# Performance work log

Hardware: AMD Instinct MI355X
Metric: run time of the kernel (lower is better)

## Reference

```python
import jax, jax.numpy as jnp
import numpy as np

B, S, E, H = 2, 2048, 2048, 16
NOPE, ROPE, VD = 128, 64, 128
QH = NOPE + ROPE  # 192
LORA = 512
ROPE_THETA = 10000.0
EPS = 1e-6


def setup_inputs() -> dict:
    key = jax.random.key(0)
    ks = jax.random.split(key, 5)
    sd = lambda n: 1.0 / np.sqrt(n)
    return {
        "x": jax.random.normal(ks[0], (B, S, E), jnp.float32),
        "wq": jax.random.normal(ks[1], (E, H * QH), jnp.float32) * sd(E),
        "wkv_a": jax.random.normal(ks[2], (E, LORA + ROPE), jnp.float32) * sd(E),
        "wkv_b": jax.random.normal(ks[3], (LORA, H * (NOPE + VD)), jnp.float32) * sd(LORA),
        "wo": jax.random.normal(ks[4], (H * VD, E), jnp.float32) * sd(H * VD),
        "kv_norm_scale": jnp.ones((LORA,), jnp.float32),
    }


def _rope(xp, cos, sin):
    # xp: (..., s, d); cos/sin: (s, d//2)
    d2 = xp.shape[-1] // 2
    x1, x2 = xp[..., :d2], xp[..., d2:]
    return jnp.concatenate([x1 * cos - x2 * sin, x2 * cos + x1 * sin], axis=-1)


def reference(x, wq, wkv_a, wkv_b, wo, kv_norm_scale):
    b, s, _ = x.shape
    # queries: (b, H, s, QH), split into no-pe / pe slices
    q = (x @ wq).reshape(b, s, H, QH).transpose(0, 2, 1, 3)
    q_nope, q_pe = q[..., :NOPE], q[..., NOPE:]

    # low-rank KV latent projection
    kva = x @ wkv_a  # (b, s, LORA + ROPE)
    ckv, k_pe = kva[..., :LORA], kva[..., LORA:]
    ckv = ckv * jax.lax.rsqrt(jnp.mean(ckv * ckv, axis=-1, keepdims=True) + EPS)
    ckv = ckv * kv_norm_scale  # RMSNorm on latent
    kv = (ckv @ wkv_b).reshape(b, s, H, NOPE + VD).transpose(0, 2, 1, 3)
    k_nope, v = kv[..., :NOPE], kv[..., NOPE:]

    # partial RoPE on the rope slice only
    pos = jnp.arange(s, dtype=jnp.float32)
    inv = 1.0 / (ROPE_THETA ** (jnp.arange(0, ROPE, 2, dtype=jnp.float32) / ROPE))
    ang = pos[:, None] * inv  # (s, ROPE//2)
    cos, sin = jnp.cos(ang), jnp.sin(ang)
    q_pe = _rope(q_pe, cos, sin)                 # (b, H, s, ROPE)
    k_pe = _rope(k_pe[:, None, :, :], cos, sin)  # (b, 1, s, ROPE), shared over heads

    # concat (the new_empty + slice-write in torch)
    qs = jnp.concatenate([q_nope, q_pe], axis=-1)  # (b, H, s, QH)
    ks_ = jnp.concatenate(
        [k_nope, jnp.broadcast_to(k_pe, (b, H, s, ROPE))], axis=-1
    )  # (b, H, s, QH)

    # causal SDPA with scale = q_head_dim**-0.5; asymmetric V head dim
    scale = QH ** -0.5
    scores = jnp.einsum('bhqd,bhkd->bhqk', qs, ks_) * scale
    causal = jnp.tril(jnp.ones((s, s), dtype=bool))
    scores = jnp.where(causal, scores, jnp.finfo(scores.dtype).min)
    attn = jax.nn.softmax(scores, axis=-1)
    out = jnp.einsum('bhqk,bhkd->bhqd', attn, v)  # (b, H, s, VD)
    out = out.transpose(0, 2, 1, 3).reshape(b, s, H * VD)
    return out @ wo
```

## Files before the change

### kernel.cpp

```cpp
#include <hip/hip_runtime.h>
#include <stdint.h>
#include <stddef.h>

typedef __bf16 bf16x8 __attribute__((ext_vector_type(8)));
typedef float floatx4 __attribute__((ext_vector_type(4)));
typedef unsigned short u16;

__device__ __forceinline__ float bf2f(u16 h) {
    unsigned u = ((unsigned)h) << 16;
    return __builtin_bit_cast(float, u);
}
__device__ __forceinline__ u16 f2bf(float f) {
    unsigned u = __builtin_bit_cast(unsigned, f);
    u += 0x7fffu + ((u >> 16) & 1u);
    return (u16)(u >> 16);
}

__device__ __forceinline__ void gload16(const void* g, void* l) {
    __builtin_amdgcn_global_load_lds(
        (const __attribute__((address_space(1))) uint32_t*)g,
        (__attribute__((address_space(3))) uint32_t*)l, 16, 0, 0);
}

__device__ __forceinline__ void wait_vm8() { asm volatile("s_waitcnt vmcnt(8)" ::: "memory"); }
__device__ __forceinline__ void wait_vm6() { asm volatile("s_waitcnt vmcnt(6)" ::: "memory"); }
__device__ __forceinline__ void wait_vm4() { asm volatile("s_waitcnt vmcnt(4)" ::: "memory"); }
__device__ __forceinline__ void wait_vm3() { asm volatile("s_waitcnt vmcnt(3)" ::: "memory"); }
__device__ __forceinline__ void wait_vm0() { asm volatile("s_waitcnt vmcnt(0)" ::: "memory"); }

__global__ __launch_bounds__(256) void k_conv_x(const float* __restrict__ in,
                                                u16* __restrict__ out, int n8) {
    int i = blockIdx.x * 256 + threadIdx.x;
    if (i >= n8) return;
    const float* f = in + (size_t)i * 8;
    unsigned o[4];
    for (int t = 0; t < 4; t++) {
        u16 lo = f2bf(f[2 * t]), hi = f2bf(f[2 * t + 1]);
        o[t] = (unsigned)lo | ((unsigned)hi << 16);
    }
    uint4 p = {o[0], o[1], o[2], o[3]};
    *(uint4*)&out[(size_t)i * 8] = p;
}

__global__ __launch_bounds__(256) void k_convT(const float* __restrict__ in,
                                               u16* __restrict__ out, int K, int N) {
    __shared__ u16 t[32][33];
    int k0 = blockIdx.x * 32, n0 = blockIdx.y * 32;
    int c = threadIdx.x & 31, r8 = threadIdx.x >> 5;
    for (int j = 0; j < 4; j++) {
        int row = r8 + j * 8;
        int n = n0 + c;
        t[row][c] = (n < N) ? f2bf(in[(size_t)(k0 + row) * N + n]) : (u16)0;
    }
    __syncthreads();
    for (int j = 0; j < 4; j++) {
        int row = r8 + j * 8;
        out[(size_t)(n0 + row) * K + k0 + c] = t[c][row];
    }
}

__global__ __launch_bounds__(256) void k_transpose_v(const u16* __restrict__ kv,
                                                     u16* __restrict__ vt) {
    __shared__ u16 t[32][33];
    int bh = blockIdx.z;
    int s0 = blockIdx.x * 32, v0 = blockIdx.y * 32;
    int c = threadIdx.x & 31, r8 = threadIdx.x >> 5;
    int b = bh >> 4, h = bh & 15;
    for (int j = 0; j < 4; j++) {
        int s = s0 + r8 + j * 8;
        t[r8 + j * 8][c] = kv[(size_t)(b * 2048 + s) * 4096 + h * 256 + 128 + v0 + c];
    }
    __syncthreads();
    for (int j = 0; j < 4; j++) {
        int v = v0 + r8 + j * 8;
        vt[((size_t)bh * 128 + v) * 2048 + s0 + c] = t[c][r8 + j * 8];
    }
}

template <bool F32OUT>
__global__ __launch_bounds__(256) void k_gemm_bt(const u16* __restrict__ A,
                                                 const u16* __restrict__ BT,
                                                 void* __restrict__ Cout,
                                                 int N, int K, int ldc) {
    __shared__ __align__(16) u16 As[128 * 32];
    __shared__ __align__(16) u16 Bs[128 * 32];
    int tid = threadIdx.x;
    int lane = tid & 63, wave = tid >> 6;
    int quad = lane >> 4, l15 = lane & 15;
    size_t m0 = (size_t)blockIdx.x * 128, n0 = (size_t)blockIdx.y * 128;
    int wm = (wave >> 1) * 64, wn = (wave & 1) * 64;
    const floatx4 fzero = {0.f, 0.f, 0.f, 0.f};
    floatx4 acc[4][4];
    for (int i = 0; i < 4; i++)
        for (int j = 0; j < 4; j++) acc[i][j] = fzero;

    for (int k0 = 0; k0 < K; k0 += 32) {
        for (int i = 0; i < 2; i++) {
            int cid = i * 256 + wave * 64 + lane;
            int row = cid >> 2, kc = cid & 3;
            gload16(&A[(m0 + row) * K + k0 + kc * 8], &As[(size_t)(i * 256 + wave * 64) * 8]);
            gload16(&BT[(n0 + row) * K + k0 + kc * 8], &Bs[(size_t)(i * 256 + wave * 64) * 8]);
        }
        __syncthreads();
        bf16x8 af[4], bfr[4];
        for (int i = 0; i < 4; i++) af[i]  = *(const bf16x8*)&As[(wm + i * 16 + l15) * 32 + quad * 8];
        for (int j = 0; j < 4; j++) bfr[j] = *(const bf16x8*)&Bs[(wn + j * 16 + l15) * 32 + quad * 8];
        for (int i = 0; i < 4; i++)
            for (int j = 0; j < 4; j++)
                acc[i][j] = __builtin_amdgcn_mfma_f32_16x16x32_bf16(af[i], bfr[j], acc[i][j], 0, 0, 0);
        __syncthreads();
    }
    for (int i = 0; i < 4; i++)
        for (int j = 0; j < 4; j++) {
            int col = (int)n0 + wn + j * 16 + l15;
            if (col >= N) continue;
            for (int r = 0; r < 4; r++) {
                size_t row = m0 + wm + i * 16 + quad * 4 + r;
                if (F32OUT) ((float*)Cout)[row * ldc + col] = acc[i][j][r];
                else        ((u16*)Cout)[row * ldc + col] = f2bf(acc[i][j][r]);
            }
        }
}

template <int NWC, bool F32OUT>
__global__ __launch_bounds__(512, 2) void k_gemm256(const u16* __restrict__ A,
                                                    const u16* __restrict__ BT,
                                                    void* __restrict__ Cout,
                                                    int K, int ldc) {
    constexpr int MFR = 16 / (8 / NWC);
    constexpr int ACH = 2;
    constexpr int BCH = NWC / 2;
    constexpr int SLOT = 8192 + NWC * 2048;
    __shared__ __align__(16) u16 RING[4][SLOT];
    int tid = threadIdx.x;
    int w = tid >> 6, lane = tid & 63;
    int l15 = lane & 15, quad = lane >> 4;
    int wr = w / NWC, wc = w % NWC;

    int gx = gridDim.x;
    int nwg = gx * gridDim.y;
    int flat = blockIdx.y * gx + blockIdx.x;
    int cpx = nwg >> 3;
    int swz = (flat & 7) * cpx + (flat >> 3);
    int bx = swz % gx, by = swz / gx;
    size_t m0 = (size_t)bx * 256, n0 = (size_t)by * (NWC * 64);
    int NT = K >> 5;

    const u16* srcA[ACH];
    const u16* srcB[BCH];
    int ldsAb[ACH], ldsBb[BCH];
#pragma unroll
    for (int p = 0; p < ACH; p++) {
        int chunk = p * 512 + tid;
        int s = chunk >> 6;
        int b = (chunk & 63) * 8;
        int bu = b ^ (((b >> 8) & 1) << 4);
        int r = bu >> 5, c = bu & 31;
        srcA[p] = A + (m0 + s * 16 + r) * (size_t)K + c;
        ldsAb[p] = (p * 512 + w * 64) * 8;
    }
#pragma unroll
    for (int p = 0; p < BCH; p++) {
        int chunk = p * 512 + tid;
        int s = chunk >> 6;
        int b = (chunk & 63) * 8;
        int bu = b ^ (((b >> 8) & 1) << 4);
        int r = bu >> 5, c = bu & 31;
        srcB[p] = BT + (n0 + s * 16 + r) * (size_t)K + c;
        ldsBb[p] = 8192 + (p * 512 + w * 64) * 8;
    }

    const int swb = (l15 * 32 + quad * 8) ^ ((l15 >> 3) << 4);

    floatx4 acc[MFR][4];
    const floatx4 fzero = {0.f, 0.f, 0.f, 0.f};
#pragma unroll
    for (int i = 0; i < MFR; i++)
#pragma unroll
        for (int j = 0; j < 4; j++) acc[i][j] = fzero;

    bf16x8 aA[MFR], bB[4];

    auto STAGE = [&](int j) {
        int rs = j & 3;
        size_t ko = (size_t)j * 32;
        u16* ring = &RING[rs][0];
#pragma unroll
        for (int p = 0; p < ACH; p++) gload16(srcA[p] + ko, ring + ldsAb[p]);
#pragma unroll
        for (int p = 0; p < BCH; p++) gload16(srcB[p] + ko, ring + ldsBb[p]);
    };
    auto READ = [&](int rs) {
        const u16* ring = &RING[rs][0];
#pragma unroll
        for (int i2 = 0; i2 < MFR; i2++)
            aA[i2] = *(const bf16x8*)&ring[(wr * MFR + i2) * 512 + swb];
#pragma unroll
        for (int j2 = 0; j2 < 4; j2++)
            bB[j2] = *(const bf16x8*)&ring[8192 + (wc * 4 + j2) * 512 + swb];
    };
    auto MMA = [&]() {
        __builtin_amdgcn_s_setprio(1);
#pragma unroll
        for (int i2 = 0; i2 < MFR; i2++)
#pragma unroll
            for (int j2 = 0; j2 < 4; j2++)
                acc[i2][j2] = __builtin_amdgcn_mfma_f32_16x16x32_bf16(
                    aA[i2], bB[j2], acc[i2][j2], 0, 0, 0);
        __builtin_amdgcn_s_setprio(0);
    };

    STAGE(0); STAGE(1); STAGE(2);

    int j = 0;
    for (; j + 3 < NT; j++) {
        if constexpr (NWC == 4) wait_vm8(); else wait_vm6();
        __builtin_amdgcn_s_barrier();
        __builtin_amdgcn_sched_barrier(0);
        READ(j & 3);
        STAGE(j + 3);
        __builtin_amdgcn_sched_barrier(0);
        MMA();
    }
    {
        if constexpr (NWC == 4) wait_vm8(); else wait_vm6();
        __builtin_amdgcn_s_barrier();
        __builtin_amdgcn_sched_barrier(0);
        READ(j & 3); MMA(); j++;
    }
    {
        if constexpr (NWC == 4) wait_vm4(); else wait_vm3();
        __builtin_amdgcn_s_barrier();
        __builtin_amdgcn_sched_barrier(0);
        READ(j & 3); MMA(); j++;
    }
    {
        wait_vm0();
        __builtin_amdgcn_s_barrier();
        __builtin_amdgcn_sched_barrier(0);
        READ(j & 3); MMA();
    }

#pragma unroll
    for (int i = 0; i < MFR; i++)
#pragma unroll
        for (int j2 = 0; j2 < 4; j2++) {
            size_t col = n0 + wc * 64 + j2 * 16 + l15;
#pragma unroll
            for (int r = 0; r < 4; r++) {
                size_t row = m0 + (size_t)wr * (MFR * 16) + i * 16 + quad * 4 + r;
                if (F32OUT) ((float*)Cout)[row * ldc + col] = acc[i][j2][r];
                else        ((u16*)Cout)[row * ldc + col] = f2bf(acc[i][j2][r]);
            }
        }
}

__global__ __launch_bounds__(64) void k_rmsnorm(const u16* __restrict__ kva,
                                                const float* __restrict__ scl,
                                                u16* __restrict__ ckv) {
    int r = blockIdx.x, lane = threadIdx.x;
    const u16* row = kva + (size_t)r * 576 + lane * 8;
    uint4 raw = *(const uint4*)row;
    unsigned w[4] = {raw.x, raw.y, raw.z, raw.w};
    float f[8];
    float ss = 0.f;
    for (int t = 0; t < 4; t++) {
        f[2 * t]     = bf2f((u16)(w[t] & 0xffffu));
        f[2 * t + 1] = bf2f((u16)(w[t] >> 16));
        ss += f[2 * t] * f[2 * t] + f[2 * t + 1] * f[2 * t + 1];
    }
    for (int off = 1; off < 64; off <<= 1) ss += __shfl_xor(ss, off, 64);
    float rs = rsqrtf(ss * (1.f / 512.f) + 1e-6f);
    unsigned o[4];
    for (int t = 0; t < 4; t++) {
        u16 lo = f2bf(f[2 * t] * rs * scl[lane * 8 + 2 * t]);
        u16 hi = f2bf(f[2 * t + 1] * rs * scl[lane * 8 + 2 * t + 1]);
        o[t] = (unsigned)lo | ((unsigned)hi << 16);
    }
    uint4 packed = {o[0], o[1], o[2], o[3]};
    *(uint4*)(ckv + (size_t)r * 512 + lane * 8) = packed;
}

__global__ __launch_bounds__(256) void k_rope(u16* __restrict__ qbuf, u16* __restrict__ kva) {
    int tid = threadIdx.x;
    int rloc = tid >> 7;
    int task = tid & 127;
    int r = blockIdx.x * 2 + rloc;
    __shared__ float cs_s[2][32], sn_s[2][32];
    if (tid < 64) {
        int rr = tid >> 5, i = tid & 31;
        int ss = (blockIdx.x * 2 + rr) & 2047;
        float freq = __expf(-0.28782313662425575f * (float)i);
        float ang = (float)ss * freq;
        float sn, cs;
        sincosf(ang, &sn, &cs);
        cs_s[rr][i] = cs; sn_s[rr][i] = sn;
    }
    __syncthreads();
    if (task < 68) {
        int rb = task >> 2, q = task & 3;
        u16* base = (rb < 16) ? qbuf + (size_t)r * 3072 + rb * 192 + 128
                              : kva + (size_t)r * 576 + 512;
        u16* p1 = base + q * 8;
        uint4 x1v = *(uint4*)p1;
        uint4 x2v = *(uint4*)(p1 + 32);
        unsigned w1[4] = {x1v.x, x1v.y, x1v.z, x1v.w};
        unsigned w2[4] = {x2v.x, x2v.y, x2v.z, x2v.w};
        unsigned o1[4], o2[4];
        for (int t2 = 0; t2 < 4; t2++) {
            float a1 = bf2f((u16)(w1[t2] & 0xffffu)), b1 = bf2f((u16)(w1[t2] >> 16));
            float a2 = bf2f((u16)(w2[t2] & 0xffffu)), b2 = bf2f((u16)(w2[t2] >> 16));
            int i0 = q * 8 + t2 * 2, i1 = i0 + 1;
            float c0 = cs_s[rloc][i0], s0 = sn_s[rloc][i0];
            float c1 = cs_s[rloc][i1], s1 = sn_s[rloc][i1];
            o1[t2] = (unsigned)f2bf(a1 * c0 - a2 * s0) | ((unsigned)f2bf(b1 * c1 - b2 * s1) << 16);
            o2[t2] = (unsigned)f2bf(a2 * c0 + a1 * s0) | ((unsigned)f2bf(b2 * c1 + b1 * s1) << 16);
        }
        uint4 y1 = {o1[0], o1[1], o1[2], o1[3]};
        uint4 y2 = {o2[0], o2[1], o2[2], o2[3]};
        *(uint4*)p1 = y1;
        *(uint4*)(p1 + 32) = y2;
    }
}

__global__ __launch_bounds__(256, 3) void k_attn(const u16* __restrict__ qbuf,
                                                 const u16* __restrict__ kv,
                                                 const u16* __restrict__ kva,
                                                 const u16* __restrict__ vt,
                                                 u16* __restrict__ attno) {
    int tid = threadIdx.x;
    int wave = tid >> 6, lane = tid & 63;
    int quad = lane >> 4, l15 = lane & 15;
    int hb = blockIdx.x;
    int h = hb & 15, b = hb >> 4;
    int qb = 31 - (int)blockIdx.y;
    int qg0 = qb * 64 + wave * 16;
    int row = qg0 + l15;

    __shared__ __align__(16) u16 Kn[2][32 * 136];
    __shared__ __align__(16) u16 Kp[2][32 * 72];
    __shared__ __align__(16) u16 Vs[2][128 * 40];
    __shared__ __align__(16) u16 P[4][16 * 40];

    const u16* qrp = qbuf + ((size_t)(b * 2048) + qg0 + l15) * 3072 + h * 192;
    bf16x8 qf[6];
    for (int c = 0; c < 6; c++) qf[c] = *(const bf16x8*)&qrp[c * 32 + quad * 8];

    const floatx4 fzero = {0.f, 0.f, 0.f, 0.f};
    floatx4 o[8];
    for (int f = 0; f < 8; f++) o[f] = fzero;
    float lp = 0.f;

    const u16* kvb = kv  + (size_t)(b * 2048) * 4096 + h * 256;
    const u16* kpb = kva + (size_t)(b * 2048) * 576 + 512;
    const u16* vtb = vt  + (size_t)(b * 16 + h) * 128 * 2048;
    const float scale = 0.07216878364870323f;

    int nkt = qb * 2 + 2;

    int kKey0 = tid >> 4,          kOff0 = (tid & 15) * 8;
    int kKey1 = (tid + 256) >> 4,  kOff1 = (tid & 15) * 8;
    int pKey  = tid >> 3,          pOff  = (tid & 7) * 8;
    int vRow0 = tid >> 2,          vOff0 = (tid & 3) * 8;
    int vRow1 = (tid + 256) >> 2,  vOff1 = (tid & 3) * 8;

    {
        uint4 a = *(const uint4*)&kvb[(size_t)kKey0 * 4096 + kOff0];
        uint4 c = *(const uint4*)&kvb[(size_t)kKey1 * 4096 + kOff1];
        uint4 d = *(const uint4*)&kpb[(size_t)pKey * 576 + pOff];
        uint4 e = *(const uint4*)&vtb[(size_t)vRow0 * 2048 + vOff0];
        uint4 g = *(const uint4*)&vtb[(size_t)vRow1 * 2048 + vOff1];
        *(uint4*)&Kn[0][kKey0 * 136 + kOff0] = a;
        *(uint4*)&Kn[0][kKey1 * 136 + kOff1] = c;
        *(uint4*)&Kp[0][pKey * 72 + pOff] = d;
        *(uint4*)&Vs[0][vRow0 * 40 + vOff0] = e;
        *(uint4*)&Vs[0][vRow1 * 40 + vOff1] = g;
    }
    __syncthreads();

    for (int kt = 0; kt < nkt; kt++) {
        int cur = kt & 1;
        bool have = (kt + 1) < nkt;
        uint4 sA = {}, sB = {}, sC = {}, sD = {}, sE = {};
        if (have) {
            int kb = (kt + 1) * 32;
            sA = *(const uint4*)&kvb[(size_t)(kb + kKey0) * 4096 + kOff0];
            sB = *(const uint4*)&kvb[(size_t)(kb + kKey1) * 4096 + kOff1];
            sC = *(const uint4*)&kpb[(size_t)(kb + pKey) * 576 + pOff];
            sD = *(const uint4*)&vtb[(size_t)vRow0 * 2048 + kb + vOff0];
            sE = *(const uint4*)&vtb[(size_t)vRow1 * 2048 + kb + vOff1];
        }
        if (kt * 32 <= qg0 + 15) {
            bf16x8 vf[8];
            for (int f = 0; f < 8; f++)
                vf[f] = *(const bf16x8*)&Vs[cur][(f * 16 + l15) * 40 + quad * 8];
            floatx4 sc[2] = {fzero, fzero};
            for (int hf = 0; hf < 2; hf++) {
                const u16* kn = &Kn[cur][(hf * 16 + l15) * 136];
                const u16* kp = &Kp[cur][(hf * 16 + l15) * 72];
                for (int c = 0; c < 4; c++) {
                    bf16x8 kf = *(const bf16x8*)&kn[c * 32 + quad * 8];
                    sc[hf] = __builtin_amdgcn_mfma_f32_16x16x32_bf16(kf, qf[c], sc[hf], 0, 0, 0);
                }
                for (int c = 0; c < 2; c++) {
                    bf16x8 kf = *(const bf16x8*)&kp[c * 32 + quad * 8];
                    sc[hf] = __builtin_amdgcn_mfma_f32_16x16x32_bf16(kf, qf[4 + c], sc[hf], 0, 0, 0);
                }
            }
            asm volatile("" ::: "memory");
            for (int hf = 0; hf < 2; hf++) {
                int keyb = kt * 32 + hf * 16 + quad * 4;
                float p[4];
                for (int r = 0; r < 4; r++)
                    p[r] = (keyb + r <= row) ? __expf(sc[hf][r] * scale) : 0.f;
                lp += (p[0] + p[1]) + (p[2] + p[3]);
                unsigned d0 = (unsigned)f2bf(p[0]) | ((unsigned)f2bf(p[1]) << 16);
                unsigned d1 = (unsigned)f2bf(p[2]) | ((unsigned)f2bf(p[3]) << 16);
                uint2 pk = {d0, d1};
                *(uint2*)&P[wave][l15 * 40 + hf * 16 + quad * 4] = pk;
            }
            asm volatile("" ::: "memory");
            bf16x8 pa = *(const bf16x8*)&P[wave][l15 * 40 + quad * 8];
            asm volatile("" ::: "memory");
            for (int f = 0; f < 8; f++)
                o[f] = __builtin_amdgcn_mfma_f32_16x16x32_bf16(pa, vf[f], o[f], 0, 0, 0);
        }
        if (have) {
            int nb = cur ^ 1;
            *(uint4*)&Kn[nb][kKey0 * 136 + kOff0] = sA;
            *(uint4*)&Kn[nb][kKey1 * 136 + kOff1] = sB;
            *(uint4*)&Kp[nb][pKey * 72 + pOff] = sC;
            *(uint4*)&Vs[nb][vRow0 * 40 + vOff0] = sD;
            *(uint4*)&Vs[nb][vRow1 * 40 + vOff1] = sE;
        }
        __syncthreads();
    }

    lp += __shfl_xor(lp, 16, 64);
    lp += __shfl_xor(lp, 32, 64);
    float lrow[4];
    for (int r = 0; r < 4; r++) lrow[r] = __shfl(lp, quad * 4 + r, 64);
    for (int f = 0; f < 8; f++)
        for (int r = 0; r < 4; r++) {
            int orow = qg0 + quad * 4 + r;
            float val = o[f][r] / lrow[r];
            attno[((size_t)(b * 2048) + orow) * 2048 + h * 128 + f * 16 + l15] = f2bf(val);
        }
}

extern "C" void kernel_launch(void* const* d_in, const int* in_sizes, int n_in,
                              void* d_out, int out_size, void* d_ws, size_t ws_size,
                              hipStream_t stream) {
    const float* x_raw    = (const float*)d_in[0];
    const float* wq_raw   = (const float*)d_in[1];
    const float* wkva_raw = (const float*)d_in[2];
    const float* wkvb_raw = (const float*)d_in[3];
    const float* wo_raw   = (const float*)d_in[4];
    const float* kvs_raw  = (const float*)d_in[5];
    float* out = (float*)d_out;
    u16* ws = (u16*)d_ws;

    const size_t O_ATT = 0;
    const size_t O_VT  = 8388608;
    const size_t O_QB  = 16777216;
    const size_t O_KVA = 29360128;
    const size_t O_KV  = 31719424;
    const size_t TOTAL_BYTES = 48496640ull * 2;
    if (ws_size < TOTAL_BYTES) return;

    u16* wq_t   = ws + O_ATT;
    u16* wkva_t = ws + O_ATT;
    u16* ckv    = ws + O_ATT;
    u16* wkvb_t = ws + O_ATT + 2097152;
    u16* attno  = ws + O_ATT;
    u16* x_bf   = ws + O_VT;
    u16* vt     = ws + O_VT;
    u16* qbuf   = ws + O_QB;
    u16* wo_t   = ws + O_QB;
    u16* kva    = ws + O_KVA;
    u16* kv     = ws + O_KV;

    k_conv_x<<<4096, 256, 0, stream>>>(x_raw, x_bf, 1048576);
    k_convT<<<dim3(64, 96), 256, 0, stream>>>(wq_raw, wq_t, 2048, 3072);

    k_gemm256<4, false><<<dim3(16, 12), 512, 0, stream>>>(x_bf, wq_t, qbuf, 2048, 3072);

    k_convT<<<dim3(64, 20), 256, 0, stream>>>(wkva_raw, wkva_t, 2048, 576);
    k_gemm_bt<false><<<dim3(32, 5), 256, 0, stream>>>(x_bf, wkva_t, kva, 576, 2048, 576);

    k_rmsnorm<<<4096, 64, 0, stream>>>(kva, kvs_raw, ckv);
    k_convT<<<dim3(16, 128), 256, 0, stream>>>(wkvb_raw, wkvb_t, 512, 4096);
    k_gemm256<4, false><<<dim3(16, 16), 512, 0, stream>>>(ckv, wkvb_t, kv, 512, 4096);

    k_rope<<<2048, 256, 0, stream>>>(qbuf, kva);
    k_transpose_v<<<dim3(64, 4, 32), 256, 0, stream>>>(kv, vt);

    k_attn<<<dim3(32, 32), 256, 0, stream>>>(qbuf, kv, kva, vt, attno);

    k_convT<<<dim3(64, 64), 256, 0, stream>>>(wo_raw, wo_t, 2048, 2048);
    k_gemm256<2, true><<<dim3(16, 16), 512, 0, stream>>>(attno, wo_t, out, 2048, 2048);
}
```

Before: 404.7 us.

## Fuse Q and KV-A projections into one GEMM; raise MFMA priority in attention

The transposed Wq and Wkv_a weights are stacked into one 3648-column B matrix. A single pipelined 256-row GEMM now produces both outputs, with an epilogue that routes columns to qbuf or kva. This drops the separate unpipelined 128-tile kernel for the KV-A projection and one launch, at the cost of running the Q part at a narrower column tile and computing a padded tail tile whose results are thrown away. Separately, the attention kernel wraps its QK and PV MFMA blocks in s_setprio so those waves get issue priority over waves doing loads and softmax.

```diff
diff --git a/kernel.cpp b/kernel.cpp
--- a/kernel.cpp
+++ b/kernel.cpp
@@ -77,55 +77,11 @@
     }
 }
 
-template <bool F32OUT>
-__global__ __launch_bounds__(256) void k_gemm_bt(const u16* __restrict__ A,
-                                                 const u16* __restrict__ BT,
-                                                 void* __restrict__ Cout,
-                                                 int N, int K, int ldc) {
-    __shared__ __align__(16) u16 As[128 * 32];
-    __shared__ __align__(16) u16 Bs[128 * 32];
-    int tid = threadIdx.x;
-    int lane = tid & 63, wave = tid >> 6;
-    int quad = lane >> 4, l15 = lane & 15;
-    size_t m0 = (size_t)blockIdx.x * 128, n0 = (size_t)blockIdx.y * 128;
-    int wm = (wave >> 1) * 64, wn = (wave & 1) * 64;
-    const floatx4 fzero = {0.f, 0.f, 0.f, 0.f};
-    floatx4 acc[4][4];
-    for (int i = 0; i < 4; i++)
-        for (int j = 0; j < 4; j++) acc[i][j] = fzero;
-
-    for (int k0 = 0; k0 < K; k0 += 32) {
-        for (int i = 0; i < 2; i++) {
-            int cid = i * 256 + wave * 64 + lane;
-            int row = cid >> 2, kc = cid & 3;
-            gload16(&A[(m0 + row) * K + k0 + kc * 8], &As[(size_t)(i * 256 + wave * 64) * 8]);
-            gload16(&BT[(n0 + row) * K + k0 + kc * 8], &Bs[(size_t)(i * 256 + wave * 64) * 8]);
-        }
-        __syncthreads();
-        bf16x8 af[4], bfr[4];
-        for (int i = 0; i < 4; i++) af[i]  = *(const bf16x8*)&As[(wm + i * 16 + l15) * 32 + quad * 8];
-        for (int j = 0; j < 4; j++) bfr[j] = *(const bf16x8*)&Bs[(wn + j * 16 + l15) * 32 + quad * 8];
-        for (int i = 0; i < 4; i++)
-            for (int j = 0; j < 4; j++)
-                acc[i][j] = __builtin_amdgcn_mfma_f32_16x16x32_bf16(af[i], bfr[j], acc[i][j], 0, 0, 0);
-        __syncthreads();
-    }
-    for (int i = 0; i < 4; i++)
-        for (int j = 0; j < 4; j++) {
-            int col = (int)n0 + wn + j * 16 + l15;
-            if (col >= N) continue;
-            for (int r = 0; r < 4; r++) {
-                size_t row = m0 + wm + i * 16 + quad * 4 + r;
-                if (F32OUT) ((float*)Cout)[row * ldc + col] = acc[i][j][r];
-                else        ((u16*)Cout)[row * ldc + col] = f2bf(acc[i][j][r]);
-            }
-        }
-}
-
-template <int NWC, bool F32OUT>
+template <int NWC, int MODE>
 __global__ __launch_bounds__(512, 2) void k_gemm256(const u16* __restrict__ A,
                                                     const u16* __restrict__ BT,
-                                                    void* __restrict__ Cout,
+                                                    void* __restrict__ C0,
+                                                    void* __restrict__ C1,
                                                     int K, int ldc) {
     constexpr int MFR = 16 / (8 / NWC);
     constexpr int ACH = 2;
@@ -249,8 +205,16 @@
 #pragma unroll
             for (int r = 0; r < 4; r++) {
                 size_t row = m0 + (size_t)wr * (MFR * 16) + i * 16 + quad * 4 + r;
-                if (F32OUT) ((float*)Cout)[row * ldc + col] = acc[i][j2][r];
-                else        ((u16*)Cout)[row * ldc + col] = f2bf(acc[i][j2][r]);
+                if constexpr (MODE == 0) {
+                    ((u16*)C0)[row * ldc + col] = f2bf(acc[i][j2][r]);
+                } else if constexpr (MODE == 1) {
+                    ((float*)C0)[row * ldc + col] = acc[i][j2][r];
+                } else {
+                    if (col < 3072)
+                        ((u16*)C0)[row * 3072 + col] = f2bf(acc[i][j2][r]);
+                    else if (col < 3648)
+                        ((u16*)C1)[row * 576 + (col - 3072)] = f2bf(acc[i][j2][r]);
+                }
             }
         }
 }
@@ -395,6 +359,7 @@
             for (int f = 0; f < 8; f++)
                 vf[f] = *(const bf16x8*)&Vs[cur][(f * 16 + l15) * 40 + quad * 8];
             floatx4 sc[2] = {fzero, fzero};
+            __builtin_amdgcn_s_setprio(1);
             for (int hf = 0; hf < 2; hf++) {
                 const u16* kn = &Kn[cur][(hf * 16 + l15) * 136];
                 const u16* kp = &Kp[cur][(hf * 16 + l15) * 72];
@@ -407,6 +372,7 @@
                     sc[hf] = __builtin_amdgcn_mfma_f32_16x16x32_bf16(kf, qf[4 + c], sc[hf], 0, 0, 0);
                 }
             }
+            __builtin_amdgcn_s_setprio(0);
             asm volatile("" ::: "memory");
             for (int hf = 0; hf < 2; hf++) {
                 int keyb = kt * 32 + hf * 16 + quad * 4;
@@ -422,8 +388,10 @@
             asm volatile("" ::: "memory");
             bf16x8 pa = *(const bf16x8*)&P[wave][l15 * 40 + quad * 8];
             asm volatile("" ::: "memory");
+            __builtin_amdgcn_s_setprio(1);
             for (int f = 0; f < 8; f++)
                 o[f] = __builtin_amdgcn_mfma_f32_16x16x32_bf16(pa, vf[f], o[f], 0, 0, 0);
+            __builtin_amdgcn_s_setprio(0);
         }
         if (have) {
             int nb = cur ^ 1;
@@ -468,8 +436,7 @@
     const size_t TOTAL_BYTES = 48496640ull * 2;
     if (ws_size < TOTAL_BYTES) return;
 
-    u16* wq_t   = ws + O_ATT;
-    u16* wkva_t = ws + O_ATT;
+    u16* g12bt  = ws + O_ATT;
     u16* ckv    = ws + O_ATT;
     u16* wkvb_t = ws + O_ATT + 2097152;
     u16* attno  = ws + O_ATT;
@@ -481,16 +448,14 @@
     u16* kv     = ws + O_KV;
 
     k_conv_x<<<4096, 256, 0, stream>>>(x_raw, x_bf, 1048576);
-    k_convT<<<dim3(64, 96), 256, 0, stream>>>(wq_raw, wq_t, 2048, 3072);
-
-    k_gemm256<4, false><<<dim3(16, 12), 512, 0, stream>>>(x_bf, wq_t, qbuf, 2048, 3072);
-
-    k_convT<<<dim3(64, 20), 256, 0, stream>>>(wkva_raw, wkva_t, 2048, 576);
-    k_gemm_bt<false><<<dim3(32, 5), 256, 0, stream>>>(x_bf, wkva_t, kva, 576, 2048, 576);
+    k_convT<<<dim3(64, 96), 256, 0, stream>>>(wq_raw, g12bt, 2048, 3072);
+    k_convT<<<dim3(64, 20), 256, 0, stream>>>(wkva_raw, g12bt + (size_t)3072 * 2048, 2048, 576);
+
+    k_gemm256<2, 2><<<dim3(16, 29), 512, 0, stream>>>(x_bf, g12bt, qbuf, kva, 2048, 0);
 
     k_rmsnorm<<<4096, 64, 0, stream>>>(kva, kvs_raw, ckv);
     k_convT<<<dim3(16, 128), 256, 0, stream>>>(wkvb_raw, wkvb_t, 512, 4096);
-    k_gemm256<4, false><<<dim3(16, 16), 512, 0, stream>>>(ckv, wkvb_t, kv, 512, 4096);
+    k_gemm256<4, 0><<<dim3(16, 16), 512, 0, stream>>>(ckv, wkvb_t, kv, nullptr, 512, 4096);
 
     k_rope<<<2048, 256, 0, stream>>>(qbuf, kva);
     k_transpose_v<<<dim3(64, 4, 32), 256, 0, stream>>>(kv, vt);
@@ -498,5 +463,5 @@
     k_attn<<<dim3(32, 32), 256, 0, stream>>>(qbuf, kv, kva, vt, attno);
 
     k_convT<<<dim3(64, 64), 256, 0, stream>>>(wo_raw, wo_t, 2048, 2048);
-    k_gemm256<2, true><<<dim3(16, 16), 512, 0, stream>>>(attno, wo_t, out, 2048, 2048);
-}
+    k_gemm256<2, 1><<<dim3(16, 16), 512, 0, stream>>>(attno, wo_t, out, nullptr, 2048, 2048);
+}
```

New measurement: 397.0 us. About the same (-1.9%).
